# Optimization experiments

Measured on AMD Instinct MI355X. Metric: run time of the kernel, lower is better.

Reference implementation:

```python
import jax, jax.numpy as jnp
import numpy as np

D_MODEL = 1024
N_HEADS = 16
D_HEAD = D_MODEL // N_HEADS
WIN = 256
NEG_INF = -1e30


def setup_inputs() -> dict:
    key = jax.random.key(0)
    k1, k2, k3 = jax.random.split(key, 3)
    B, L = 4, 4096
    x = jax.random.normal(k1, (B, L, D_MODEL), dtype=jnp.float32)
    w_qkv = jax.random.normal(k2, (D_MODEL, 3 * D_MODEL), dtype=jnp.float32) * (1.0 / np.sqrt(D_MODEL))
    w_out = jax.random.normal(k3, (D_MODEL, D_MODEL), dtype=jnp.float32) * (1.0 / np.sqrt(D_MODEL))
    return {"x": x, "w_qkv": w_qkv, "w_out": w_out}


def _band_mask(nb: int):
    ti = jnp.arange(WIN)[:, None]
    tj = jnp.arange(2 * WIN)[None, :]
    base = (tj >= ti + 1) & (tj <= ti + WIN)
    first = base & (tj >= WIN)                         # block 0 has zero-padded (invalid) prev block
    rest = jnp.broadcast_to(base, (nb - 1, WIN, 2 * WIN))
    return jnp.concatenate([first[None], rest], axis=0)


def reference(x, w_qkv, w_out):
    B, L, D = x.shape
    nb = L // WIN
    qkv = (x @ w_qkv).reshape(B, L, 3, N_HEADS, D_HEAD)
    q, k, v = qkv[:, :, 0], qkv[:, :, 1], qkv[:, :, 2]          # [B, L, H, dh]
    def to_blocks(t):
        return t.transpose(0, 2, 1, 3).reshape(B, N_HEADS, nb, WIN, D_HEAD)
    qb, kb, vb = to_blocks(q), to_blocks(k), to_blocks(v)
    zero_blk = jnp.zeros_like(kb[:, :, :1])
    k_kv = jnp.concatenate([jnp.concatenate([zero_blk, kb[:, :, :-1]], axis=2), kb], axis=3)  # [B,H,nb,2W,dh]
    v_kv = jnp.concatenate([jnp.concatenate([zero_blk, vb[:, :, :-1]], axis=2), vb], axis=3)
    scale = 1.0 / np.sqrt(D_HEAD)
    scores = jnp.einsum('bhnqd,bhnkd->bhnqk', qb, k_kv) * scale
    scores = jnp.where(_band_mask(nb), scores, NEG_INF)
    attn = jax.nn.softmax(scores, axis=-1)
    ob = jnp.einsum('bhnqk,bhnkd->bhnqd', attn, v_kv)
    out = ob.reshape(B, N_HEADS, L, D_HEAD).transpose(0, 2, 1, 3).reshape(B, L, D)
    return out @ w_out
```

## Files before the change

### kernel.cpp

```cpp
#include <hip/hip_runtime.h>

typedef __bf16 bf16_t;
typedef __bf16 bf16x8 __attribute__((ext_vector_type(8)));
typedef float f32x4 __attribute__((ext_vector_type(4)));
typedef unsigned short ushort_t;

#define MFMA_16x16x32(a, b, c) __builtin_amdgcn_mfma_f32_16x16x32_bf16((a), (b), (c), 0, 0, 0)

__device__ __forceinline__ void async_ld16(const void* gptr, void* lptr) {
  typedef __attribute__((address_space(1))) const unsigned int as1_t;
  typedef __attribute__((address_space(3))) unsigned int as3_t;
  __builtin_amdgcn_global_load_lds((as1_t*)(unsigned long long)gptr,
                                   (as3_t*)(unsigned int)(unsigned long long)lptr,
                                   16, 0, 0);
}

__global__ void detect_dtype(const ushort_t* __restrict__ x, int* __restrict__ flag) {
  __shared__ int cnt[256];
  int c = 0;
#pragma unroll
  for (int i = 0; i < 16; ++i) {
    const ushort_t u = x[threadIdx.x * 16 + i];
    const int e = (u >> 7) & 0xFF;
    if ((u & 0x7FFF) != 0 && (e < 0x3A || e > 0xC0)) ++c;
  }
  cnt[threadIdx.x] = c;
  __syncthreads();
  if (threadIdx.x == 0) {
    int t = 0;
    for (int i = 0; i < 256; ++i) t += cnt[i];
    *flag = (t > 512) ? 1 : 0;
  }
}

__global__ __launch_bounds__(256) void convert_to_bf16(const void* __restrict__ src,
                                                       bf16_t* __restrict__ dst, int n8,
                                                       const int* __restrict__ flag) {
  const int isF32 = *flag;
  int i = blockIdx.x * 256 + threadIdx.x;
  const int stride = gridDim.x * 256;
  if (isF32) {
    const float4* s = (const float4*)src;
    for (; i < n8; i += stride) {
      const float4 a = s[(size_t)i * 2];
      const float4 b = s[(size_t)i * 2 + 1];
      bf16x8 o;
      o[0] = (bf16_t)a.x; o[1] = (bf16_t)a.y; o[2] = (bf16_t)a.z; o[3] = (bf16_t)a.w;
      o[4] = (bf16_t)b.x; o[5] = (bf16_t)b.y; o[6] = (bf16_t)b.z; o[7] = (bf16_t)b.w;
      *(bf16x8*)(dst + (size_t)i * 8) = o;
    }
  } else {
    const uint4* s = (const uint4*)src;
    for (; i < n8; i += stride) ((uint4*)dst)[i] = s[i];
  }
}

__global__ __launch_bounds__(256) void transpose_cvt(const void* __restrict__ in,
                                                     ushort_t* __restrict__ out,
                                                     int R, int C,
                                                     const int* __restrict__ flag) {
  __shared__ alignas(16) ushort_t t[64 * 72];
  const int tid = threadIdx.x;
  const int c0 = blockIdx.x * 64;
  const int r0 = blockIdx.y * 64;
  if (*flag) {
    const float* s = (const float*)in;
#pragma unroll
    for (int it = 0; it < 4; ++it) {
      int cid = tid + it * 256;
      int row = cid >> 4, ch = (cid & 15) * 4;
      const float4 v = *(const float4*)(s + (size_t)(r0 + row) * C + c0 + ch);
      ushort_t* tp = t + row * 72 + ch;
      tp[0] = (ushort_t)__builtin_bit_cast(unsigned short, (bf16_t)v.x);
      tp[1] = (ushort_t)__builtin_bit_cast(unsigned short, (bf16_t)v.y);
      tp[2] = (ushort_t)__builtin_bit_cast(unsigned short, (bf16_t)v.z);
      tp[3] = (ushort_t)__builtin_bit_cast(unsigned short, (bf16_t)v.w);
    }
  } else {
    const ushort_t* s = (const ushort_t*)in;
#pragma unroll
    for (int it = 0; it < 2; ++it) {
      int cid = tid + it * 256;
      int row = cid >> 3, co = (cid & 7) * 8;
      *(uint4*)(t + row * 72 + co) = *(const uint4*)(s + (size_t)(r0 + row) * C + c0 + co);
    }
  }
  __syncthreads();
#pragma unroll
  for (int it = 0; it < 2; ++it) {
    int cid = tid + it * 256;
    int orow = cid >> 3, ko = (cid & 7) * 8;
    uint4 u;
    ushort_t* tp = (ushort_t*)&u;
#pragma unroll
    for (int j = 0; j < 8; ++j) tp[j] = t[(ko + j) * 72 + orow];
    *(uint4*)(out + (size_t)(c0 + orow) * R + r0 + ko) = u;
  }
}

__device__ __forceinline__ void gemm_core(const bf16_t* __restrict__ A, int lda,
                                          const bf16_t* __restrict__ Bt,
                                          void* __restrict__ Cout, int N_out, int K,
                                          const int* __restrict__ flag,
                                          bf16_t* __restrict__ vT) {
  __shared__ alignas(16) bf16_t smem[49152];
  const int tid = threadIdx.x;
  const int wave = tid >> 6;
  const int lane = tid & 63;
  const int l15 = lane & 15;
  const int quad = lane >> 4;
  const int wm = wave >> 2;
  const int wn = wave & 3;

  int lin = blockIdx.y * gridDim.x + blockIdx.x;
  const int nwg = gridDim.x * gridDim.y;
  if ((nwg & 7) == 0) lin = (lin & 7) * (nwg >> 3) + (lin >> 3);
  const int tn = (lin % gridDim.x) * 256;
  const int tm = (lin / gridDim.x) * 256;

  f32x4 acc[8][4];
#pragma unroll
  for (int i = 0; i < 8; ++i)
#pragma unroll
    for (int j = 0; j < 4; ++j) acc[i][j] = (f32x4){0.f, 0.f, 0.f, 0.f};

  const int r_st = tid >> 2;
  const int csrc = ((tid & 3) ^ ((tid >> 3) & 3)) * 8;
  const int wofs = wave * 512;

  const int rowA = wm * 16 + l15;
  const int rowB = wn * 16 + l15;
  const int cfr = (quad ^ ((l15 >> 1) & 3)) * 8;

  const int NT = K >> 5;

#define STAGE_HALF(G, ldg, grow0, kk, base)                                  \
  async_ld16((G) + (size_t)((grow0) + r_st) * (ldg) + (kk) + csrc,           \
             &smem[(base) + wofs])

#define STAGE4(kk, base)                                \
  do {                                                  \
    STAGE_HALF(A, lda, tm, (kk), (base));               \
    STAGE_HALF(Bt, K, tn, (kk), (base) + 8192);         \
    STAGE_HALF(Bt, K, tn + 128, (kk), (base) + 12288);  \
    STAGE_HALF(A, lda, tm + 128, (kk), (base) + 4096);  \
  } while (0)

  STAGE4(0, 0);
  STAGE4(32, 16384);
  asm volatile("s_waitcnt vmcnt(4)" ::: "memory");
  __builtin_amdgcn_s_barrier();

  int rb = 0;
  for (int t = 0; t < NT; ++t) {
    const int kst = (t + 2) << 5;
    const bool pf = (kst < K);
    const int sb = (rb >= 16384) ? rb - 16384 : rb + 32768;
    if (pf) STAGE4(kst, sb);

    bf16x8 a_[8], b_[4];
#pragma unroll
    for (int mh = 0; mh < 2; ++mh)
#pragma unroll
      for (int q = 0; q < 4; ++q)
        a_[mh * 4 + q] = *(const bf16x8*)&smem[rb + mh * 4096 +
                                               ((q * 32 + rowA) << 5) + cfr];
#pragma unroll
    for (int nh = 0; nh < 2; ++nh)
#pragma unroll
      for (int jn = 0; jn < 2; ++jn)
        b_[nh * 2 + jn] = *(const bf16x8*)&smem[rb + 8192 + nh * 4096 +
                                                ((jn * 64 + rowB) << 5) + cfr];

    __builtin_amdgcn_s_setprio(1);
#pragma unroll
    for (int f = 0; f < 8; ++f)
#pragma unroll
      for (int n = 0; n < 4; ++n) acc[f][n] = MFMA_16x16x32(a_[f], b_[n], acc[f][n]);
    __builtin_amdgcn_s_setprio(0);

    asm volatile("s_waitcnt vmcnt(4)" ::: "memory");
    if (!pf) asm volatile("s_waitcnt vmcnt(0)" ::: "memory");
    __builtin_amdgcn_s_barrier();
    rb = (rb == 32768) ? 0 : rb + 16384;
  }

  __syncthreads();

  const int isF32 = flag ? *flag : 0;
  if (isF32) {
#pragma unroll
    for (int f = 0; f < 8; ++f) {
      const int m0 = tm + (f >> 2) * 128 + (f & 3) * 32 + wm * 16 + quad * 4;
#pragma unroll
      for (int nidx = 0; nidx < 4; ++nidx) {
        const int col = tn + (nidx >> 1) * 128 + (nidx & 1) * 64 + wn * 16 + l15;
        float* cp = (float*)Cout + (size_t)m0 * N_out + col;
#pragma unroll
        for (int r = 0; r < 4; ++r) cp[(size_t)r * N_out] = acc[f][nidx][r];
      }
    }
  } else if (vT != nullptr && tn >= 2048) {
    const int bb = tm >> 12;
    const int pbase = tm & 4095;
    bf16_t* stg = smem;
#pragma unroll
    for (int g = 0; g < 4; ++g) {
      __syncthreads();
      const int colp = wn * 16 + l15;
#pragma unroll
      for (int f = 0; f < 8; ++f) {
        const int posl = (f >> 2) * 128 + (f & 3) * 32 + wm * 16 + quad * 4;
#pragma unroll
        for (int r = 0; r < 4; ++r)
          stg[colp * 264 + posl + r] = (bf16_t)acc[f][g][r];
      }
      __syncthreads();
      const int colr = tid >> 3;
      const int p0 = (tid & 7) * 32;
      const int cg = tn - 2048 + (g >> 1) * 128 + ((g & 1) << 6) + colr;
      bf16_t* dst = vT + ((size_t)(bb * 1024 + cg)) * 4096 + pbase + p0;
      const bf16_t* srcp = stg + colr * 264 + p0;
#pragma unroll
      for (int k = 0; k < 4; ++k)
        *(uint4*)(dst + k * 8) = *(const uint4*)(srcp + k * 8);
    }
  } else {
    bf16_t* stg = smem + wave * 1152;
#pragma unroll
    for (int f = 0; f < 8; ++f) {
#pragma unroll
      for (int nidx = 0; nidx < 4; ++nidx)
#pragma unroll
        for (int r = 0; r < 4; ++r)
          stg[(quad * 4 + r) * 72 + nidx * 16 + l15] = (bf16_t)acc[f][nidx][r];
      __asm__ volatile("s_waitcnt lgkmcnt(0)" ::: "memory");
      const int m0 = tm + (f >> 2) * 128 + (f & 3) * 32 + wm * 16;
#pragma unroll
      for (int p = 0; p < 2; ++p) {
        const int idx = lane + p * 64;
        const int row = idx >> 3, c8 = (idx & 7) * 8;
        uint4 u = *(const uint4*)(stg + row * 72 + c8);
        const int col = tn + ((c8 >> 5) << 7) + (((c8 >> 4) & 1) << 6) + wn * 16 + (c8 & 15);
        *(uint4*)((bf16_t*)Cout + (size_t)(m0 + row) * N_out + col) = u;
      }
      __asm__ volatile("s_waitcnt lgkmcnt(0)" ::: "memory");
    }
  }
#undef STAGE_HALF
#undef STAGE4
}

__global__ __launch_bounds__(512) void gemm_qkv(const bf16_t* __restrict__ A, int lda,
                                                const bf16_t* __restrict__ Bt,
                                                void* __restrict__ Cout, int N_out,
                                                int K, bf16_t* __restrict__ vT) {
  gemm_core(A, lda, Bt, Cout, N_out, K, nullptr, vT);
}
__global__ __launch_bounds__(512) void gemm_outp(const bf16_t* __restrict__ A, int lda,
                                                 const bf16_t* __restrict__ Bt,
                                                 void* __restrict__ Cout, int N_out,
                                                 int K, const int* __restrict__ flag) {
  gemm_core(A, lda, Bt, Cout, N_out, K, flag, nullptr);
}

__global__ __launch_bounds__(256) void attn_swa(bf16_t* qkv, const bf16_t* __restrict__ vT) {
  __shared__ alignas(16) bf16_t k_lds[64 * 72];
  __shared__ alignas(16) bf16_t vt_lds[64 * 72];
  __shared__ alignas(16) bf16_t p_lds[4 * 16 * 72];

  int wg = blockIdx.x;
  wg = (wg & 7) * 512 + (wg >> 3);
  const int b = wg >> 10;
  const int h = (wg >> 6) & 15;
  const int qt = wg & 63;
  const int blk = qt >> 2;
  const int wq = qt & 3;
  const int tid = threadIdx.x;
  const int wave = tid >> 6;
  const int lane = tid & 63;
  const int l15 = lane & 15;
  const int quad = lane >> 4;
  const int qw = qt * 64 + wave * 16;

  const size_t qoff = ((size_t)(b * 4096 + qw + l15)) * 3072 + h * 64;
  const bf16x8 qf0 = *(const bf16x8*)(qkv + qoff + quad * 8);
  const bf16x8 qf1 = *(const bf16x8*)(qkv + qoff + 32 + quad * 8);

  f32x4 of[4];
#pragma unroll
  for (int i = 0; i < 4; ++i) of[i] = (f32x4){0.f, 0.f, 0.f, 0.f};
  float m_i[4], l_i[4];
#pragma unroll
  for (int r = 0; r < 4; ++r) {
    m_i[r] = -1e30f;
    l_i[r] = 0.0f;
  }

  const int kb0 = blk * 256 - 256;
  const int kclo = (blk == 0) ? 4 : wq;
  const int kchi = wq + 4;

  const int row0 = tid >> 3;
  const int co8 = (tid & 7) * 8;
  const bf16_t* kbase = qkv + ((size_t)b * 4096) * 3072 + 1024 + h * 64;
  const bf16_t* vbase = vT + (((size_t)b * 16 + h) * 64) * 4096;
  uint4 kr0, kr1, vr0, vr1;

#define ISSUE_KV(KB)                                                           \
  do {                                                                         \
    kr0 = *(const uint4*)(kbase + (size_t)((KB) + row0) * 3072 + co8);         \
    kr1 = *(const uint4*)(kbase + (size_t)((KB) + row0 + 32) * 3072 + co8);    \
    vr0 = *(const uint4*)(vbase + (size_t)row0 * 4096 + (KB) + co8);           \
    vr1 = *(const uint4*)(vbase + (size_t)(row0 + 32) * 4096 + (KB) + co8);    \
  } while (0)

  ISSUE_KV(kb0 + kclo * 64);

  for (int kc = kclo; kc <= kchi; ++kc) {
    const int kb = kb0 + kc * 64;
    __syncthreads();
    *(uint4*)(k_lds + row0 * 72 + co8) = kr0;
    *(uint4*)(k_lds + (row0 + 32) * 72 + co8) = kr1;
    *(uint4*)(vt_lds + row0 * 72 + co8) = vr0;
    *(uint4*)(vt_lds + (row0 + 32) * 72 + co8) = vr1;
    if (kc < kchi) ISSUE_KV(kb + 64);
    __syncthreads();

    f32x4 s[4];
    __builtin_amdgcn_s_setprio(1);
#pragma unroll
    for (int nt = 0; nt < 4; ++nt) {
      bf16x8 kf0 = *(const bf16x8*)(k_lds + (nt * 16 + l15) * 72 + quad * 8);
      bf16x8 kf1 = *(const bf16x8*)(k_lds + (nt * 16 + l15) * 72 + 32 + quad * 8);
      f32x4 z = (f32x4){0.f, 0.f, 0.f, 0.f};
      z = MFMA_16x16x32(qf0, kf0, z);
      z = MFMA_16x16x32(qf1, kf1, z);
      s[nt] = z;
    }
    __builtin_amdgcn_s_setprio(0);

    float sv[4][4];
#pragma unroll
    for (int nt = 0; nt < 4; ++nt) {
      const int key = kb + nt * 16 + l15;
#pragma unroll
      for (int r = 0; r < 4; ++r) {
        const int p = qw + quad * 4 + r;
        const bool valid = (key <= p) && (key + 256 > p);
        sv[nt][r] = valid ? s[nt][r] * 0.125f : -1e30f;
      }
    }
    float rm[4];
#pragma unroll
    for (int r = 0; r < 4; ++r)
      rm[r] = fmaxf(fmaxf(sv[0][r], sv[1][r]), fmaxf(sv[2][r], sv[3][r]));
#pragma unroll
    for (int off = 1; off < 16; off <<= 1)
#pragma unroll
      for (int r = 0; r < 4; ++r) rm[r] = fmaxf(rm[r], __shfl_xor(rm[r], off));

    float mn[4], alpha[4];
#pragma unroll
    for (int r = 0; r < 4; ++r) {
      mn[r] = fmaxf(m_i[r], rm[r]);
      alpha[r] = __expf(m_i[r] - mn[r]);
      m_i[r] = mn[r];
    }

    float rs[4] = {0.f, 0.f, 0.f, 0.f};
#pragma unroll
    for (int nt = 0; nt < 4; ++nt)
#pragma unroll
      for (int r = 0; r < 4; ++r) {
        const float pv = (sv[nt][r] > -1e29f) ? __expf(sv[nt][r] - mn[r]) : 0.0f;
        rs[r] += pv;
        p_lds[wave * 1152 + (quad * 4 + r) * 72 + nt * 16 + l15] = (bf16_t)pv;
      }
#pragma unroll
    for (int off = 1; off < 16; off <<= 1)
#pragma unroll
      for (int r = 0; r < 4; ++r) rs[r] += __shfl_xor(rs[r], off);
#pragma unroll
    for (int r = 0; r < 4; ++r) l_i[r] = l_i[r] * alpha[r] + rs[r];
#pragma unroll
    for (int dt = 0; dt < 4; ++dt)
#pragma unroll
      for (int r = 0; r < 4; ++r) of[dt][r] *= alpha[r];

    __builtin_amdgcn_s_setprio(1);
#pragma unroll
    for (int kk = 0; kk < 2; ++kk) {
      bf16x8 pf = *(const bf16x8*)(p_lds + wave * 1152 + l15 * 72 + kk * 32 + quad * 8);
#pragma unroll
      for (int dt = 0; dt < 4; ++dt) {
        bf16x8 vf = *(const bf16x8*)(vt_lds + (dt * 16 + l15) * 72 + kk * 32 + quad * 8);
        of[dt] = MFMA_16x16x32(pf, vf, of[dt]);
      }
    }
    __builtin_amdgcn_s_setprio(0);
  }
#undef ISSUE_KV

  float inv[4];
#pragma unroll
  for (int r = 0; r < 4; ++r) inv[r] = 1.0f / fmaxf(l_i[r], 1e-20f);
  bf16_t* op = qkv + ((size_t)(b * 4096 + qw)) * 3072 + h * 64;
#pragma unroll
  for (int dt = 0; dt < 4; ++dt)
#pragma unroll
    for (int r = 0; r < 4; ++r)
      op[(size_t)(quad * 4 + r) * 3072 + dt * 16 + l15] = (bf16_t)(of[dt][r] * inv[r]);
}

extern "C" void kernel_launch(void* const* d_in, const int* in_sizes, int n_in,
                              void* d_out, int out_size, void* d_ws, size_t ws_size,
                              hipStream_t stream) {
  char* ws = (char*)d_ws;
  bf16_t* wTq = (bf16_t*)(ws);
  bf16_t* wTo = (bf16_t*)(ws + 6291456);
  bf16_t* qkv = (bf16_t*)(ws + 8388608);
  int* flag = (int*)(ws + 109051904);

  bf16_t* xb = (bf16_t*)d_out;
  bf16_t* vTb = (bf16_t*)((char*)d_out + 33554432);

  detect_dtype<<<1, 256, 0, stream>>>((const ushort_t*)d_in[0], flag);
  convert_to_bf16<<<1024, 256, 0, stream>>>(d_in[0], xb, 2097152, flag);
  transpose_cvt<<<dim3(48, 16), 256, 0, stream>>>(d_in[1], (ushort_t*)wTq, 1024, 3072,
                                                  flag);
  transpose_cvt<<<dim3(16, 16), 256, 0, stream>>>(d_in[2], (ushort_t*)wTo, 1024, 1024,
                                                  flag);
  gemm_qkv<<<dim3(12, 64), 512, 0, stream>>>(xb, 1024, wTq, qkv, 3072, 1024, vTb);
  attn_swa<<<dim3(4096), 256, 0, stream>>>(qkv, vTb);
  gemm_outp<<<dim3(4, 64), 512, 0, stream>>>(qkv, 3072, wTo, d_out, 1024, 1024, flag);
}
```

Before: 356.7 us.

## Process 128 queries per attention block and batch V-transpose epilogue stores

Each attention workgroup now handles 128 query rows, two 16-row groups per wave, instead of 64. Every K/V tile loaded into LDS is reused across twice as many queries, so K/V global traffic and the number of workgroups are halved. The cost is a wider KV range per block (up to 6 chunks of 64 keys, more of them partly masked), higher register pressure, and a larger P buffer in LDS. Separately, the QKV GEMM's V-transpose epilogue writes packed bf16 pairs and stages two column groups per barrier pair, halving the syncthreads there.

Result: slower. 369.7 us (+3.6%).

```diff
diff --git a/kernel.cpp b/kernel.cpp
--- a/kernel.cpp
+++ b/kernel.cpp
@@ -13,6 +13,12 @@
   __builtin_amdgcn_global_load_lds((as1_t*)(unsigned long long)gptr,
                                    (as3_t*)(unsigned int)(unsigned long long)lptr,
                                    16, 0, 0);
+}
+
+__device__ __forceinline__ unsigned int pack_bf16x2(float a, float b) {
+  unsigned int lo = __builtin_bit_cast(unsigned short, (bf16_t)a);
+  unsigned int hi = __builtin_bit_cast(unsigned short, (bf16_t)b);
+  return lo | (hi << 16);
 }
 
 __global__ void detect_dtype(const ushort_t* __restrict__ x, int* __restrict__ flag) {
@@ -204,26 +210,36 @@
     const int bb = tm >> 12;
     const int pbase = tm & 4095;
     bf16_t* stg = smem;
-#pragma unroll
-    for (int g = 0; g < 4; ++g) {
+    const int colp = wn * 16 + l15;
+    const int colr = tid >> 3;
+    const int p0 = (tid & 7) * 32;
+#pragma unroll
+    for (int gp = 0; gp < 2; ++gp) {
       __syncthreads();
-      const int colp = wn * 16 + l15;
-#pragma unroll
-      for (int f = 0; f < 8; ++f) {
-        const int posl = (f >> 2) * 128 + (f & 3) * 32 + wm * 16 + quad * 4;
-#pragma unroll
-        for (int r = 0; r < 4; ++r)
-          stg[colp * 264 + posl + r] = (bf16_t)acc[f][g][r];
+#pragma unroll
+      for (int half = 0; half < 2; ++half) {
+        const int g = gp * 2 + half;
+        bf16_t* tile = stg + half * 16896;
+#pragma unroll
+        for (int f = 0; f < 8; ++f) {
+          const int posl = (f >> 2) * 128 + (f & 3) * 32 + wm * 16 + quad * 4;
+          uint2 u;
+          u.x = pack_bf16x2(acc[f][g][0], acc[f][g][1]);
+          u.y = pack_bf16x2(acc[f][g][2], acc[f][g][3]);
+          *(uint2*)(tile + colp * 264 + posl) = u;
+        }
       }
       __syncthreads();
-      const int colr = tid >> 3;
-      const int p0 = (tid & 7) * 32;
-      const int cg = tn - 2048 + (g >> 1) * 128 + ((g & 1) << 6) + colr;
-      bf16_t* dst = vT + ((size_t)(bb * 1024 + cg)) * 4096 + pbase + p0;
-      const bf16_t* srcp = stg + colr * 264 + p0;
-#pragma unroll
-      for (int k = 0; k < 4; ++k)
-        *(uint4*)(dst + k * 8) = *(const uint4*)(srcp + k * 8);
+#pragma unroll
+      for (int half = 0; half < 2; ++half) {
+        const int g = gp * 2 + half;
+        const int cg = tn - 2048 + (g >> 1) * 128 + ((g & 1) << 6) + colr;
+        const bf16_t* srcp = stg + half * 16896 + colr * 264 + p0;
+        bf16_t* dst = vT + ((size_t)(bb * 1024 + cg)) * 4096 + pbase + p0;
+#pragma unroll
+        for (int k = 0; k < 4; ++k)
+          *(uint4*)(dst + k * 8) = *(const uint4*)(srcp + k * 8);
+      }
     }
   } else {
     bf16_t* stg = smem + wave * 1152;
@@ -267,39 +283,45 @@
 __global__ __launch_bounds__(256) void attn_swa(bf16_t* qkv, const bf16_t* __restrict__ vT) {
   __shared__ alignas(16) bf16_t k_lds[64 * 72];
   __shared__ alignas(16) bf16_t vt_lds[64 * 72];
-  __shared__ alignas(16) bf16_t p_lds[4 * 16 * 72];
+  __shared__ alignas(16) bf16_t p_lds[4 * 2 * 16 * 72];
 
   int wg = blockIdx.x;
-  wg = (wg & 7) * 512 + (wg >> 3);
-  const int b = wg >> 10;
-  const int h = (wg >> 6) & 15;
-  const int qt = wg & 63;
-  const int blk = qt >> 2;
-  const int wq = qt & 3;
+  wg = (wg & 7) * 256 + (wg >> 3);
+  const int b = wg >> 9;
+  const int h = (wg >> 5) & 15;
+  const int qt = wg & 31;
   const int tid = threadIdx.x;
   const int wave = tid >> 6;
   const int lane = tid & 63;
   const int l15 = lane & 15;
   const int quad = lane >> 4;
-  const int qw = qt * 64 + wave * 16;
-
-  const size_t qoff = ((size_t)(b * 4096 + qw + l15)) * 3072 + h * 64;
-  const bf16x8 qf0 = *(const bf16x8*)(qkv + qoff + quad * 8);
-  const bf16x8 qf1 = *(const bf16x8*)(qkv + qoff + 32 + quad * 8);
-
-  f32x4 of[4];
-#pragma unroll
-  for (int i = 0; i < 4; ++i) of[i] = (f32x4){0.f, 0.f, 0.f, 0.f};
-  float m_i[4], l_i[4];
-#pragma unroll
-  for (int r = 0; r < 4; ++r) {
-    m_i[r] = -1e30f;
-    l_i[r] = 0.0f;
-  }
-
-  const int kb0 = blk * 256 - 256;
-  const int kclo = (blk == 0) ? 4 : wq;
-  const int kchi = wq + 4;
+  const int qw = qt * 128 + wave * 32;
+
+  bf16x8 qf[2][2];
+#pragma unroll
+  for (int rg = 0; rg < 2; ++rg) {
+    const size_t qoff = ((size_t)(b * 4096 + qw + rg * 16 + l15)) * 3072 + h * 64;
+    qf[rg][0] = *(const bf16x8*)(qkv + qoff + quad * 8);
+    qf[rg][1] = *(const bf16x8*)(qkv + qoff + 32 + quad * 8);
+  }
+
+  f32x4 of[2][4];
+#pragma unroll
+  for (int rg = 0; rg < 2; ++rg)
+#pragma unroll
+    for (int i = 0; i < 4; ++i) of[rg][i] = (f32x4){0.f, 0.f, 0.f, 0.f};
+  float m_i[2][4], l_i[2][4];
+#pragma unroll
+  for (int rg = 0; rg < 2; ++rg)
+#pragma unroll
+    for (int r = 0; r < 4; ++r) {
+      m_i[rg][r] = -1e30f;
+      l_i[rg][r] = 0.0f;
+    }
+
+  const int kb0 = qt * 128 - 256;
+  const int kclo = (qt == 0) ? 4 : ((qt == 1) ? 2 : 0);
+  const int kchi = 5;
 
   const int row0 = tid >> 3;
   const int co8 = (tid & 7) * 8;
@@ -327,90 +349,117 @@
     if (kc < kchi) ISSUE_KV(kb + 64);
     __syncthreads();
 
-    f32x4 s[4];
+    f32x4 s[2][4];
     __builtin_amdgcn_s_setprio(1);
 #pragma unroll
     for (int nt = 0; nt < 4; ++nt) {
       bf16x8 kf0 = *(const bf16x8*)(k_lds + (nt * 16 + l15) * 72 + quad * 8);
       bf16x8 kf1 = *(const bf16x8*)(k_lds + (nt * 16 + l15) * 72 + 32 + quad * 8);
-      f32x4 z = (f32x4){0.f, 0.f, 0.f, 0.f};
-      z = MFMA_16x16x32(qf0, kf0, z);
-      z = MFMA_16x16x32(qf1, kf1, z);
-      s[nt] = z;
+#pragma unroll
+      for (int rg = 0; rg < 2; ++rg) {
+        f32x4 z = (f32x4){0.f, 0.f, 0.f, 0.f};
+        z = MFMA_16x16x32(qf[rg][0], kf0, z);
+        z = MFMA_16x16x32(qf[rg][1], kf1, z);
+        s[rg][nt] = z;
+      }
     }
     __builtin_amdgcn_s_setprio(0);
 
-    float sv[4][4];
+    float sv[2][4][4];
 #pragma unroll
     for (int nt = 0; nt < 4; ++nt) {
       const int key = kb + nt * 16 + l15;
 #pragma unroll
+      for (int rg = 0; rg < 2; ++rg)
+#pragma unroll
+        for (int r = 0; r < 4; ++r) {
+          const int p = qw + rg * 16 + quad * 4 + r;
+          const bool valid = (key <= p) && (key + 256 > p);
+          sv[rg][nt][r] = valid ? s[rg][nt][r] * 0.125f : -1e30f;
+        }
+    }
+    float rm[2][4];
+#pragma unroll
+    for (int rg = 0; rg < 2; ++rg)
+#pragma unroll
+      for (int r = 0; r < 4; ++r)
+        rm[rg][r] = fmaxf(fmaxf(sv[rg][0][r], sv[rg][1][r]),
+                          fmaxf(sv[rg][2][r], sv[rg][3][r]));
+#pragma unroll
+    for (int off = 1; off < 16; off <<= 1)
+#pragma unroll
+      for (int rg = 0; rg < 2; ++rg)
+#pragma unroll
+        for (int r = 0; r < 4; ++r) rm[rg][r] = fmaxf(rm[rg][r], __shfl_xor(rm[rg][r], off));
+
+    float mn[2][4], alpha[2][4];
+#pragma unroll
+    for (int rg = 0; rg < 2; ++rg)
+#pragma unroll
       for (int r = 0; r < 4; ++r) {
-        const int p = qw + quad * 4 + r;
-        const bool valid = (key <= p) && (key + 256 > p);
-        sv[nt][r] = valid ? s[nt][r] * 0.125f : -1e30f;
-      }
-    }
-    float rm[4];
-#pragma unroll
-    for (int r = 0; r < 4; ++r)
-      rm[r] = fmaxf(fmaxf(sv[0][r], sv[1][r]), fmaxf(sv[2][r], sv[3][r]));
+        mn[rg][r] = fmaxf(m_i[rg][r], rm[rg][r]);
+        alpha[rg][r] = __expf(m_i[rg][r] - mn[rg][r]);
+        m_i[rg][r] = mn[rg][r];
+      }
+
+    float rs[2][4] = {{0.f, 0.f, 0.f, 0.f}, {0.f, 0.f, 0.f, 0.f}};
+#pragma unroll
+    for (int nt = 0; nt < 4; ++nt)
+#pragma unroll
+      for (int rg = 0; rg < 2; ++rg)
+#pragma unroll
+        for (int r = 0; r < 4; ++r) {
+          const float pv = (sv[rg][nt][r] > -1e29f) ? __expf(sv[rg][nt][r] - mn[rg][r]) : 0.0f;
+          rs[rg][r] += pv;
+          p_lds[(wave * 2 + rg) * 1152 + (quad * 4 + r) * 72 + nt * 16 + l15] = (bf16_t)pv;
+        }
 #pragma unroll
     for (int off = 1; off < 16; off <<= 1)
 #pragma unroll
-      for (int r = 0; r < 4; ++r) rm[r] = fmaxf(rm[r], __shfl_xor(rm[r], off));
-
-    float mn[4], alpha[4];
-#pragma unroll
-    for (int r = 0; r < 4; ++r) {
-      mn[r] = fmaxf(m_i[r], rm[r]);
-      alpha[r] = __expf(m_i[r] - mn[r]);
-      m_i[r] = mn[r];
-    }
-
-    float rs[4] = {0.f, 0.f, 0.f, 0.f};
-#pragma unroll
-    for (int nt = 0; nt < 4; ++nt)
-#pragma unroll
-      for (int r = 0; r < 4; ++r) {
-        const float pv = (sv[nt][r] > -1e29f) ? __expf(sv[nt][r] - mn[r]) : 0.0f;
-        rs[r] += pv;
-        p_lds[wave * 1152 + (quad * 4 + r) * 72 + nt * 16 + l15] = (bf16_t)pv;
-      }
-#pragma unroll
-    for (int off = 1; off < 16; off <<= 1)
-#pragma unroll
-      for (int r = 0; r < 4; ++r) rs[r] += __shfl_xor(rs[r], off);
-#pragma unroll
-    for (int r = 0; r < 4; ++r) l_i[r] = l_i[r] * alpha[r] + rs[r];
+      for (int rg = 0; rg < 2; ++rg)
+#pragma unroll
+        for (int r = 0; r < 4; ++r) rs[rg][r] += __shfl_xor(rs[rg][r], off);
+#pragma unroll
+    for (int rg = 0; rg < 2; ++rg)
+#pragma unroll
+      for (int r = 0; r < 4; ++r) l_i[rg][r] = l_i[rg][r] * alpha[rg][r] + rs[rg][r];
+#pragma unroll
+    for (int rg = 0; rg < 2; ++rg)
+#pragma unroll
+      for (int dt = 0; dt < 4; ++dt)
+#pragma unroll
+        for (int r = 0; r < 4; ++r) of[rg][dt][r] *= alpha[rg][r];
+
+    __builtin_amdgcn_s_setprio(1);
+#pragma unroll
+    for (int kk = 0; kk < 2; ++kk) {
+#pragma unroll
+      for (int rg = 0; rg < 2; ++rg) {
+        bf16x8 pf = *(const bf16x8*)(p_lds + (wave * 2 + rg) * 1152 + l15 * 72 +
+                                     kk * 32 + quad * 8);
+#pragma unroll
+        for (int dt = 0; dt < 4; ++dt) {
+          bf16x8 vf = *(const bf16x8*)(vt_lds + (dt * 16 + l15) * 72 + kk * 32 + quad * 8);
+          of[rg][dt] = MFMA_16x16x32(pf, vf, of[rg][dt]);
+        }
+      }
+    }
+    __builtin_amdgcn_s_setprio(0);
+  }
+#undef ISSUE_KV
+
+#pragma unroll
+  for (int rg = 0; rg < 2; ++rg) {
+    float inv[4];
+#pragma unroll
+    for (int r = 0; r < 4; ++r) inv[r] = 1.0f / fmaxf(l_i[rg][r], 1e-20f);
+    bf16_t* op = qkv + ((size_t)(b * 4096 + qw + rg * 16)) * 3072 + h * 64;
 #pragma unroll
     for (int dt = 0; dt < 4; ++dt)
 #pragma unroll
-      for (int r = 0; r < 4; ++r) of[dt][r] *= alpha[r];
-
-    __builtin_amdgcn_s_setprio(1);
-#pragma unroll
-    for (int kk = 0; kk < 2; ++kk) {
-      bf16x8 pf = *(const bf16x8*)(p_lds + wave * 1152 + l15 * 72 + kk * 32 + quad * 8);
-#pragma unroll
-      for (int dt = 0; dt < 4; ++dt) {
-        bf16x8 vf = *(const bf16x8*)(vt_lds + (dt * 16 + l15) * 72 + kk * 32 + quad * 8);
-        of[dt] = MFMA_16x16x32(pf, vf, of[dt]);
-      }
-    }
-    __builtin_amdgcn_s_setprio(0);
-  }
-#undef ISSUE_KV
-
-  float inv[4];
-#pragma unroll
-  for (int r = 0; r < 4; ++r) inv[r] = 1.0f / fmaxf(l_i[r], 1e-20f);
-  bf16_t* op = qkv + ((size_t)(b * 4096 + qw)) * 3072 + h * 64;
-#pragma unroll
-  for (int dt = 0; dt < 4; ++dt)
-#pragma unroll
-    for (int r = 0; r < 4; ++r)
-      op[(size_t)(quad * 4 + r) * 3072 + dt * 16 + l15] = (bf16_t)(of[dt][r] * inv[r]);
+      for (int r = 0; r < 4; ++r)
+        op[(size_t)(quad * 4 + r) * 3072 + dt * 16 + l15] = (bf16_t)(of[rg][dt][r] * inv[r]);
+  }
 }
 
 extern "C" void kernel_launch(void* const* d_in, const int* in_sizes, int n_in,
@@ -432,6 +481,6 @@
   transpose_cvt<<<dim3(16, 16), 256, 0, stream>>>(d_in[2], (ushort_t*)wTo, 1024, 1024,
                                                   flag);
   gemm_qkv<<<dim3(12, 64), 512, 0, stream>>>(xb, 1024, wTq, qkv, 3072, 1024, vTb);
-  attn_swa<<<dim3(4096), 256, 0, stream>>>(qkv, vTb);
+  attn_swa<<<dim3(2048), 256, 0, stream>>>(qkv, vTb);
   gemm_outp<<<dim3(4, 64), 512, 0, stream>>>(qkv, 3072, wTo, d_out, 1024, 1024, flag);
 }
```
